# Kernel optimization log

Hardware: AMD Instinct MI355X
Metric: run time of the kernel (lower is better)

## Reference

```python
import jax, jax.numpy as jnp
import numpy as np

IMG_SIZE = 224
ALPHA = 100.0  # hardcoded softmax temperature in knnsearch_t_grad


def _sqdist(a, b):
    # (B,N,C),(B,M,C) -> (B,N,M) squared euclidean distances
    return (jnp.sum(a * a, -1)[:, :, None]
            - 2.0 * jnp.einsum('bnc,bmc->bnm', a, b)
            + jnp.sum(b * b, -1)[:, None, :])


def _cdist(a, b):
    return jnp.sqrt(jnp.maximum(_sqdist(a, b), 1e-12))


def proj2img(pc, img_offset):
    # faithful jax port of GraphDeformLoss_Neural_Partial.proj2img
    B, N, _ = pc.shape
    pc_max = pc.max(axis=1)              # (B,3)
    pc_min_full = pc.min(axis=1)         # (B,3)
    pc_range = pc_max - pc_min_full
    grid_size = pc_range[:, :2].max(axis=-1) / (IMG_SIZE - 3)   # (B,)
    pc_min = pc_min_full[:, None, :2]                            # (B,1,2)
    gs = grid_size[:, None, None]
    idx_xy = jnp.floor((pc[:, :, :2] - pc_min) / gs)             # (B,N,2)
    # densify each point into a 5x5 neighborhood of pixels
    idx_dense = (idx_xy[:, :, None, :] + img_offset[None, None]).reshape(B, N * 25, 2) + 1.0
    center = jnp.floor((idx_dense.max(axis=1) + idx_dense.min(axis=1)) / 2.0)  # (B,2)
    offset = IMG_SIZE / 2.0 - center - 1.0                       # (B,2) = (offset_x, offset_y)
    idx_off = idx_dense + offset[:, None, :]
    # boundary correction as in the torch code, plus clip for safety
    idx_off = idx_off + (idx_off < 0).astype(jnp.float32) - (idx_off > IMG_SIZE - 1).astype(jnp.float32)
    idx_off = jnp.clip(idx_off, 0, IMG_SIZE - 1)
    f_dense = jnp.repeat(jnp.repeat(pc[:, :, None, 2:3], 25, axis=2).reshape(B, N * 25, 1), 3, axis=-1)
    flat = (idx_off[..., 0] * IMG_SIZE + idx_off[..., 1]).astype(jnp.int32)   # (B,N*25)
    out = jax.vmap(lambda f, i: jax.ops.segment_sum(f, i, num_segments=IMG_SIZE * IMG_SIZE))(f_dense, flat)
    img = out.reshape(B, IMG_SIZE, IMG_SIZE, 3).transpose(0, 3, 1, 2)  # (B,3,H,W)
    return jax.nn.sigmoid(img)


def setup_inputs() -> dict:
    key = jax.random.key(0)
    k1, k2, k3, k4 = jax.random.split(key, 4)
    B, N, M, C = 4, 4995, 4995, 128
    off = jnp.array([[i, j] for i in range(-2, 3) for j in range(-2, 3)], dtype=jnp.float32)
    return {
        'verts1': jax.random.normal(k1, (B, N, 3), jnp.float32),
        'verts2': jax.random.normal(k2, (B, M, 3), jnp.float32),
        'feat1': jax.random.normal(k3, (B, N, C), jnp.float32),
        'feat2': jax.random.normal(k4, (B, M, C), jnp.float32),
        'img_offset': off,
        'k': 10,
    }


def reference(verts1, verts2, feat1, feat2, img_offset, k):
    # knnsearch_t_grad: soft correspondence from feature-space cdist + softmax
    d_feat = _cdist(feat1, feat2)                               # (B,N,M)
    Pi_12 = jax.nn.softmax(-ALPHA * d_feat, axis=-1)
    verts12 = jnp.einsum('bnm,bmc->bnc', Pi_12, verts2)         # pulled-back points (B,N,3)
    # chamfer (squared distances, as chamfer_3DDist); partial: take dist1 branch (N<=M)
    d2 = _sqdist(verts12, verts2)
    self_rec_loss = jnp.mean(jnp.min(d2, axis=-1))
    # knn_grad + index_points: gather k-NN features on source cloud
    d2_11 = _sqdist(verts1, verts1)
    _, idx11 = jax.lax.top_k(-d2_11, k)                         # (B,N,k) nearest
    feat1_conv = jax.vmap(lambda p, i: p[i])(feat1, idx11)      # (B,N,k,C)
    deform_feat_loss = jnp.mean((feat1_conv - feat1[:, :, None, :]) ** 2)
    # point-to-image projection loss
    img1 = proj2img(verts12, img_offset)
    img2 = proj2img(verts2, img_offset)
    img_loss = jnp.mean((img1 - img2) ** 2)
    return self_rec_loss + img_loss + deform_feat_loss
```

## Files before the change

### kernel.cpp

```cpp
#include <hip/hip_runtime.h>
#include <math.h>

#define BB 4
#define NN 4995
#define CC 128
#define IMG 224
#define IMGP (IMG*IMG)
#define ALPHA_F 100.0f
#define SPLITS 6
#define COLS_PER_SPLIT 896
#define RBLK 40
#define NG 158
#define NGP 160
#define NCP 5120
#define NTAP (2*BB*NN*25)
#define NREP 4
#define TKCAP 256

#define SM_SCALE 20813.6898f
#define NEG2S   -41627.3796f
#define EPS_S    2.08136898e-8f

#define OFF_V12    0
#define OFF_FN1    60000
#define OFF_V1Q    81000
#define OFF_V2Q    161000
#define OFF_C2Q    241000
#define OFF_PART   323000
#define OFF_IMG1   1123000
#define OFF_IMG2   1323704
#define OFF_ACC    1524408
#define OFF_STATS  1524792
#define OFF_F2H    1525000
#define OFF_F2L    2820000
#define OFF_IMGR   4115000
#define WS_NEED_REP ((size_t)5721000*sizeof(float))
#define ZERO_START OFF_IMG1
#define ZERO_FLOATS (1524920 - OFF_IMG1)
#define ZERO2_FLOATS (1524920 - OFF_ACC)

typedef short v8s  __attribute__((ext_vector_type(8)));
typedef float v16f __attribute__((ext_vector_type(16)));

#if __has_builtin(__builtin_amdgcn_exp2f)
__device__ __forceinline__ float fast_exp2(float x){ return __builtin_amdgcn_exp2f(x); }
#else
__device__ __forceinline__ float fast_exp2(float x){ float r; asm("v_exp_f32 %0, %1" : "=v"(r) : "v"(x)); return r; }
#endif
#if __has_builtin(__builtin_amdgcn_sqrtf)
__device__ __forceinline__ float fast_sqrt(float x){ return __builtin_amdgcn_sqrtf(x); }
#else
__device__ __forceinline__ float fast_sqrt(float x){ float r; asm("v_sqrt_f32 %0, %1" : "=v"(r) : "v"(x)); return r; }
#endif

__device__ __forceinline__ float wave_min(float v){
#pragma unroll
  for (int off=32; off; off>>=1) v = fminf(v, __shfl_xor(v, off));
  return v;
}
__device__ __forceinline__ float wave_sum(float v){
#pragma unroll
  for (int off=32; off; off>>=1) v += __shfl_xor(v, off);
  return v;
}

__device__ __forceinline__ int pack_bf_hi(float a, float b){
  return (int)__builtin_amdgcn_perm(__float_as_uint(b), __float_as_uint(a), 0x07060302u);
}

__device__ __forceinline__ void cvt_hilo(float4 a, float4 c, int4& hi, int4& lo){
  float hx=__uint_as_float(__float_as_uint(a.x)&0xffff0000u);
  float hy=__uint_as_float(__float_as_uint(a.y)&0xffff0000u);
  float hz=__uint_as_float(__float_as_uint(a.z)&0xffff0000u);
  float hw=__uint_as_float(__float_as_uint(a.w)&0xffff0000u);
  float gx=__uint_as_float(__float_as_uint(c.x)&0xffff0000u);
  float gy=__uint_as_float(__float_as_uint(c.y)&0xffff0000u);
  float gz=__uint_as_float(__float_as_uint(c.z)&0xffff0000u);
  float gw=__uint_as_float(__float_as_uint(c.w)&0xffff0000u);
  hi = make_int4(pack_bf_hi(a.x,a.y), pack_bf_hi(a.z,a.w),
                 pack_bf_hi(c.x,c.y), pack_bf_hi(c.z,c.w));
  lo = make_int4(pack_bf_hi(a.x-hx,a.y-hy), pack_bf_hi(a.z-hz,a.w-hw),
                 pack_bf_hi(c.x-gx,c.y-gy), pack_bf_hi(c.z-gz,c.w-gw));
}

__device__ __forceinline__ v8s i4_to_s8(int4 v){
  union { int4 i; v8s s; } u; u.i = v; return u.s;
}

__device__ __forceinline__ void gld_lds16(const void* g, void* l){
  __builtin_amdgcn_global_load_lds((const __attribute__((address_space(1))) void*)g,
                                   (__attribute__((address_space(3))) void*)l, 16, 0, 0);
}

__device__ __forceinline__ unsigned int fkey(float f){
  unsigned int u = __float_as_uint(f);
  return ((int)u < 0) ? ~u : (u ^ 0x80000000u);
}

__global__ __launch_bounds__(256) void k_conv(const float* __restrict__ feat1,
                                              const float* __restrict__ feat2,
                                              const float* __restrict__ verts1,
                                              const float* __restrict__ verts2,
                                              float* __restrict__ ws) {
  __shared__ float s2p[8][32], s1p[8][32];
  int g = blockIdx.x, b = blockIdx.y;
  int t = threadIdx.x;
  if (g >= NG){
    if (t < 32){
      int c = g*32 + t;
      if (c < NCP)
        ((float4*)(ws+OFF_C2Q))[(size_t)b*NCP + c] = make_float4(0.f,0.f,0.f,1e30f);
    }
    return;
  }
  int q = t >> 5, c32 = t & 31;
  int col = g*32 + c32; if (col > NN-1) col = NN-1;
  const float4* src = (const float4*)(feat2 + ((size_t)(b*NN + col))*CC) + q*4;
  float4 v0 = src[0], v1 = src[1], v2 = src[2], v3 = src[3];
  {
    float s2 = 0.f;
    s2=fmaf(v0.x,v0.x,s2); s2=fmaf(v0.y,v0.y,s2); s2=fmaf(v0.z,v0.z,s2); s2=fmaf(v0.w,v0.w,s2);
    s2=fmaf(v1.x,v1.x,s2); s2=fmaf(v1.y,v1.y,s2); s2=fmaf(v1.z,v1.z,s2); s2=fmaf(v1.w,v1.w,s2);
    s2=fmaf(v2.x,v2.x,s2); s2=fmaf(v2.y,v2.y,s2); s2=fmaf(v2.z,v2.z,s2); s2=fmaf(v2.w,v2.w,s2);
    s2=fmaf(v3.x,v3.x,s2); s2=fmaf(v3.y,v3.y,s2); s2=fmaf(v3.z,v3.z,s2); s2=fmaf(v3.w,v3.w,s2);
    s2p[q][c32] = s2;
  }
  {
    const float4* fa = (const float4*)(feat1 + ((size_t)(b*NN + col))*CC) + q*4;
    float4 u0 = fa[0], u1 = fa[1], u2 = fa[2], u3 = fa[3];
    float s1 = 0.f;
    s1=fmaf(u0.x,u0.x,s1); s1=fmaf(u0.y,u0.y,s1); s1=fmaf(u0.z,u0.z,s1); s1=fmaf(u0.w,u0.w,s1);
    s1=fmaf(u1.x,u1.x,s1); s1=fmaf(u1.y,u1.y,s1); s1=fmaf(u1.z,u1.z,s1); s1=fmaf(u1.w,u1.w,s1);
    s1=fmaf(u2.x,u2.x,s1); s1=fmaf(u2.y,u2.y,s1); s1=fmaf(u2.z,u2.z,s1); s1=fmaf(u2.w,u2.w,s1);
    s1=fmaf(u3.x,u3.x,s1); s1=fmaf(u3.y,u3.y,s1); s1=fmaf(u3.z,u3.z,s1); s1=fmaf(u3.w,u3.w,s1);
    s1p[q][c32] = s1;
  }
  short* f2h = (short*)(ws + OFF_F2H);
  short* f2l = (short*)(ws + OFF_F2L);
  size_t base = ((size_t)(b*NG + g))*4096 + (size_t)q*512 + c32*8;
  int4 hi, lo;
  cvt_hilo(v0, v1, hi, lo);
  *(int4*)&f2h[base] = hi;  *(int4*)&f2l[base] = lo;
  cvt_hilo(v2, v3, hi, lo);
  *(int4*)&f2h[base + 256] = hi;  *(int4*)&f2l[base + 256] = lo;
  __syncthreads();
  if (t < 32){
    int c = g*32 + t;
    if (c < NN){
      float S2 = ((s2p[0][t]+s2p[1][t])+(s2p[2][t]+s2p[3][t]))
               + ((s2p[4][t]+s2p[5][t])+(s2p[6][t]+s2p[7][t]));
      float S1 = ((s1p[0][t]+s1p[1][t])+(s1p[2][t]+s1p[3][t]))
               + ((s1p[4][t]+s1p[5][t])+(s1p[6][t]+s1p[7][t]));
      size_t r = (size_t)(b*NN + c);
      float x=verts1[r*3], y=verts1[r*3+1], z=verts1[r*3+2];
      ((float4*)(ws+OFF_V1Q))[r] = make_float4(x,y,z, x*x+y*y+z*z);
      float x2=verts2[r*3], y2=verts2[r*3+1], z2=verts2[r*3+2];
      ((float4*)(ws+OFF_V2Q))[r] = make_float4(x2,y2,z2, x2*x2+y2*y2+z2*z2);
      ((float4*)(ws+OFF_C2Q))[(size_t)b*NCP + c] = make_float4(x2,y2,z2, SM_SCALE*S2);
      ws[OFF_FN1+r] = SM_SCALE*S1;
    } else if (c < NCP){
      ((float4*)(ws+OFF_C2Q))[(size_t)b*NCP + c] = make_float4(0.f,0.f,0.f,1e30f);
    }
  }
}

__global__ __launch_bounds__(256) void k_stageA(const float* __restrict__ feat1,
      float* __restrict__ ws) {
  __shared__ __align__(16) short Bbuf[2][4096];
  __shared__ __align__(16) float colq[1024*4];

  int rblk  = blockIdx.x;
  int split = blockIdx.y;
  int b     = blockIdx.z;
  int rowBase = rblk*128;
  int colBase = split*COLS_PER_SPLIT;
  int colEnd  = colBase + COLS_PER_SPLIT; if (colEnd > NN) colEnd = NN;
  int nct = (colEnd - colBase + 63) >> 6;
  int nst = nct << 2;

  int t    = threadIdx.x;
  int w    = t >> 6;
  int lane = t & 63;
  int half = lane >> 5;
  int m32  = lane & 31;

  const float* f1b = feat1 + (size_t)b*NN*CC;
  const short* f2h = (const short*)(ws + OFF_F2H);
  const short* f2l = (const short*)(ws + OFF_F2L);
  const float4* cqb = (const float4*)(ws + OFF_C2Q) + (size_t)b*NCP;

#pragma unroll
  for (int r=0; r<4; r++){
    int col = colBase + r*256 + t; if (col > NCP-1) col = NCP-1;
    gld_lds16(cqb + col, &colq[(r*256 + w*64)*4]);
  }

  size_t f2base = (((size_t)(b*NG) + (colBase>>5) + (w>>1)) << 12) + (size_t)((t&127)*8);

  {
    short* d = &Bbuf[0][0] + w*512;
    gld_lds16(f2h + f2base, d);
    gld_lds16(f2l + f2base, d + 2048);
  }

  int nrow = rowBase + w*32 + m32;
  int nclamp = nrow > NN-1 ? NN-1 : nrow;
  float sn = ws[OFF_FN1 + (size_t)b*NN + nclamp];
  const float4* ar = (const float4*)(f1b + (size_t)nclamp*CC) + (half<<1);
  v8s Afh[8], Afl[8];
#pragma unroll
  for (int sl=0; sl<8; ++sl){
    float4 v0 = ar[sl*4], v1 = ar[sl*4+1];
    int4 hi, lo;
    cvt_hilo(v0, v1, hi, lo);
    Afh[sl] = i4_to_s8(hi); Afl[sl] = i4_to_s8(lo);
  }

  __syncthreads();

  float mm = INFINITY, S = 0.f, Vx = 0.f, Vy = 0.f, Vz = 0.f;

  for (int ci = 0; ci < nct; ci++){
    v16f acc0, acc1;
#pragma unroll
    for (int i=0;i<16;i++){ acc0[i]=0.f; acc1[i]=0.f; }

#pragma unroll
    for (int kt = 0; kt < 4; kt++){
      int s = (ci<<2) + kt;
      if (s+1 < nst){
        int s1 = s+1;
        size_t so = f2base + ((size_t)(s1>>2)<<13) + ((size_t)(s1&3)<<10);
        short* d = &Bbuf[0][0] + ((s1&1)<<12) + w*512;
        gld_lds16(f2h + so, d);
        gld_lds16(f2l + so, d + 2048);
      }
      const short* Bh = &Bbuf[0][0] + ((s&1)<<12);
      const short* Bl = Bh + 2048;
#pragma unroll
      for (int kh=0; kh<2; kh++){
        int fo = (kh<<9) + (half<<8) + (m32<<3);
        v8s a0h = *(const v8s*)&Bh[fo];
        v8s a0l = *(const v8s*)&Bl[fo];
        v8s a1h = *(const v8s*)&Bh[1024+fo];
        v8s a1l = *(const v8s*)&Bl[1024+fo];
        v8s b1h = Afh[kt*2+kh];
        v8s b1l = Afl[kt*2+kh];
        __builtin_amdgcn_s_setprio(1);
        acc0 = __builtin_amdgcn_mfma_f32_32x32x16_bf16(a0h, b1h, acc0, 0,0,0);
        acc0 = __builtin_amdgcn_mfma_f32_32x32x16_bf16(a0h, b1l, acc0, 0,0,0);
        acc0 = __builtin_amdgcn_mfma_f32_32x32x16_bf16(a0l, b1h, acc0, 0,0,0);
        acc1 = __builtin_amdgcn_mfma_f32_32x32x16_bf16(a1h, b1h, acc1, 0,0,0);
        acc1 = __builtin_amdgcn_mfma_f32_32x32x16_bf16(a1h, b1l, acc1, 0,0,0);
        acc1 = __builtin_amdgcn_mfma_f32_32x32x16_bf16(a1l, b1h, acc1, 0,0,0);
        __builtin_amdgcn_s_setprio(0);
      }
      __syncthreads();
    }

    int cb4 = ci<<8;
    float Mt = INFINITY;
#pragma unroll
    for (int reg=0; reg<16; reg++){
      int cp0 = (reg&3) + 8*(reg>>2) + 4*half;
      float f0 = colq[cb4 + cp0*4 + 3];
      float d0 = fmaf(NEG2S, acc0[reg], sn) + f0;
      float p0 = fast_sqrt(fmaxf(d0, EPS_S));
      acc0[reg] = p0; Mt = fminf(Mt, p0);
      float f1v = colq[cb4 + (cp0+32)*4 + 3];
      float d1 = fmaf(NEG2S, acc1[reg], sn) + f1v;
      float p1 = fast_sqrt(fmaxf(d1, EPS_S));
      acc1[reg] = p1; Mt = fminf(Mt, p1);
    }
    float mn = fminf(mm, Mt);
    float sc = fast_exp2(mn - mm);
    float se=0.f, sx=0.f, sy=0.f, sz=0.f;
#pragma unroll
    for (int reg=0; reg<16; reg++){
      int cp0 = (reg&3) + 8*(reg>>2) + 4*half;
      float4 q0 = *(const float4*)&colq[cb4 + cp0*4];
      float e0 = fast_exp2(mn - acc0[reg]);
      se += e0; sx=fmaf(e0,q0.x,sx); sy=fmaf(e0,q0.y,sy); sz=fmaf(e0,q0.z,sz);
      float4 q1 = *(const float4*)&colq[cb4 + (cp0+32)*4];
      float e1 = fast_exp2(mn - acc1[reg]);
      se += e1; sx=fmaf(e1,q1.x,sx); sy=fmaf(e1,q1.y,sy); sz=fmaf(e1,q1.z,sz);
    }
    S  = fmaf(S,  sc, se);
    Vx = fmaf(Vx, sc, sx);
    Vy = fmaf(Vy, sc, sy);
    Vz = fmaf(Vz, sc, sz);
    mm = mn;
  }

  {
    float m2  = __shfl_xor(mm, 32);
    float S2  = __shfl_xor(S,  32);
    float Vx2 = __shfl_xor(Vx, 32);
    float Vy2 = __shfl_xor(Vy, 32);
    float Vz2 = __shfl_xor(Vz, 32);
    float M = fminf(mm, m2);
    float c1 = fast_exp2(M - mm), c2 = fast_exp2(M - m2);
    float Sf  = S*c1  + S2*c2;
    float Vxf = Vx*c1 + Vx2*c2;
    float Vyf = Vy*c1 + Vy2*c2;
    float Vzf = Vz*c1 + Vz2*c2;
    if (half==0 && nrow < NN){
      float* p = ws + OFF_PART + ((size_t)(b*NN+nrow)*SPLITS + split)*5;
      p[0]=M; p[1]=Sf; p[2]=Vxf; p[3]=Vyf; p[4]=Vzf;
    }
  }
}

__global__ __launch_bounds__(256) void k_selfrec(float* __restrict__ ws) {
  __shared__ float v12s[32][3];
  int rblk = blockIdx.x, b = blockIdx.y;
  int t = threadIdx.x;
  int lane = t & 63, w = t >> 6;
  int r0blk = rblk*32;

  if (t < 32){
    int row = r0blk + t;
    int rowc = row > NN-1 ? NN-1 : row;
    const float* p = ws + OFF_PART + (size_t)(b*NN+rowc)*SPLITS*5;
    float mm = INFINITY;
#pragma unroll
    for (int s=0;s<SPLITS;s++) mm = fminf(mm, p[s*5]);
    float S=0.f,Vx=0.f,Vy=0.f,Vz=0.f;
#pragma unroll
    for (int s=0;s<SPLITS;s++){
      float sc = fast_exp2(mm - p[s*5]);
      S  += p[s*5+1]*sc; Vx += p[s*5+2]*sc; Vy += p[s*5+3]*sc; Vz += p[s*5+4]*sc;
    }
    float ox = Vx/S, oy = Vy/S, oz = Vz/S;
    v12s[t][0]=ox; v12s[t][1]=oy; v12s[t][2]=oz;
    if (row < NN){
      ws[OFF_V12+(size_t)(b*NN+row)*3+0]=ox;
      ws[OFF_V12+(size_t)(b*NN+row)*3+1]=oy;
      ws[OFF_V12+(size_t)(b*NN+row)*3+2]=oz;
    }
  }
  __syncthreads();

  int r0 = r0blk + w*8;
  const float4* v2q = (const float4*)(ws + OFF_V2Q) + (size_t)b*NN;
  float xr[8], yr[8], zr[8], sar[8]; bool val[8];
#pragma unroll
  for (int j=0;j<8;j++){
    int n = r0+j; val[j] = (n < NN);
    int li = w*8+j;
    float x=v12s[li][0], y=v12s[li][1], z=v12s[li][2];
    sar[j]=x*x+y*y+z*z;
    xr[j]=-2.0f*x; yr[j]=-2.0f*y; zr[j]=-2.0f*z;
  }
  float mn[8];
#pragma unroll
  for (int j=0;j<8;j++) mn[j] = INFINITY;
  for (int m=lane; m<NN; m+=64) {
    float4 q = v2q[m];
#pragma unroll
    for (int j=0;j<8;j++)
      mn[j] = fminf(mn[j], fmaf(xr[j],q.x, fmaf(yr[j],q.y, fmaf(zr[j],q.z, q.w))));
  }
  float s = 0.f;
#pragma unroll
  for (int j=0;j<8;j++){
    float v = wave_min(mn[j]);
    s += val[j] ? (v + sar[j]) : 0.f;
  }
  if (lane==0)
    atomicAdd(((double*)(ws+OFF_ACC)) + ((rblk*4 + w) & 63), (double)s);
}

__global__ __launch_bounds__(256) void k_topk(const float* __restrict__ feat1,
        const int* __restrict__ kptr, float* __restrict__ ws) {
  __shared__ unsigned int keybuf[4*256];
  __shared__ unsigned long long cand[4*TKCAP];
  __shared__ int scnt[4];
  __shared__ float tfs[4];
  __shared__ int sel[4][16];
  __shared__ float rs[4];
  int t = threadIdx.x;
  int lane = t & 63, wid = t >> 6;
  int b = blockIdx.y;
  int n0 = blockIdx.x*4;
  int kk = *kptr; if (kk > 16) kk = 16; if (kk < 1) kk = 1;

  const float4* v1q = (const float4*)(ws + OFF_V1Q) + (size_t)b*NN;
  float mx[4], my2[4], mz[4];
#pragma unroll
  for (int j=0;j<4;j++){
    int n = n0+j; if (n > NN-1) n = NN-1;
    float4 me = v1q[n];
    mx[j]=-2.0f*me.x; my2[j]=-2.0f*me.y; mz[j]=-2.0f*me.z;
  }
  if (t < 4) scnt[t] = 0;

  float mn[4] = {INFINITY, INFINITY, INFINITY, INFINITY};
  for (int i=0;i<20;i++){
    int m = t + 256*i;
    if (m < NN){
      float4 q = v1q[m];
#pragma unroll
      for (int j=0;j<4;j++){
        float d = fmaf(mx[j], q.x, fmaf(my2[j], q.y, fmaf(mz[j], q.z, q.w)));
        mn[j] = fminf(mn[j], d);
      }
    }
  }

#pragma unroll
  for (int j=0;j<4;j++)
    keybuf[j*256 + t] = fkey(mn[j]) >> 16;
  __syncthreads();

  {
    unsigned int k0 = keybuf[wid*256 + lane];
    unsigned int k1 = keybuf[wid*256 + 64 + lane];
    unsigned int k2 = keybuf[wid*256 + 128 + lane];
    unsigned int k3 = keybuf[wid*256 + 192 + lane];
    unsigned int prefix = 0;
    for (int bit=15; bit>=0; --bit){
      unsigned int piv = prefix | (1u<<bit);
      int c = __popcll(__ballot(k0 < piv)) + __popcll(__ballot(k1 < piv))
            + __popcll(__ballot(k2 < piv)) + __popcll(__ballot(k3 < piv));
      if (c < kk) prefix = piv;
    }
    unsigned int K = (prefix<<16) | 0xFFFFu;
    unsigned int fb = (K & 0x80000000u) ? (K ^ 0x80000000u) : ~K;
    if (lane==0) tfs[wid] = __uint_as_float(fb);
  }
  __syncthreads();
  float tf0 = tfs[0], tf1 = tfs[1], tf2 = tfs[2], tf3 = tfs[3];

  bool g0 = (mn[0] <= tf0), g1 = (mn[1] <= tf1), g2 = (mn[2] <= tf2), g3 = (mn[3] <= tf3);
  if (g0|g1|g2|g3){
    for (int i=0;i<20;i++){
      int m = t + 256*i;
      if (m < NN){
        float4 q = v1q[m];
        float sw = q.w;
        float d0 = fmaf(mx[0], q.x, fmaf(my2[0], q.y, fmaf(mz[0], q.z, sw)));
        float d1 = fmaf(mx[1], q.x, fmaf(my2[1], q.y, fmaf(mz[1], q.z, sw)));
        float d2 = fmaf(mx[2], q.x, fmaf(my2[2], q.y, fmaf(mz[2], q.z, sw)));
        float d3 = fmaf(mx[3], q.x, fmaf(my2[3], q.y, fmaf(mz[3], q.z, sw)));
        if (g0 && d0 <= tf0){
          int pos = atomicAdd(&scnt[0], 1);
          if (pos < TKCAP) cand[0*TKCAP + pos] = ((unsigned long long)fkey(d0) << 13) | (unsigned int)m;
        }
        if (g1 && d1 <= tf1){
          int pos = atomicAdd(&scnt[1], 1);
          if (pos < TKCAP) cand[1*TKCAP + pos] = ((unsigned long long)fkey(d1) << 13) | (unsigned int)m;
        }
        if (g2 && d2 <= tf2){
          int pos = atomicAdd(&scnt[2], 1);
          if (pos < TKCAP) cand[2*TKCAP + pos] = ((unsigned long long)fkey(d2) << 13) | (unsigned int)m;
        }
        if (g3 && d3 <= tf3){
          int pos = atomicAdd(&scnt[3], 1);
          if (pos < TKCAP) cand[3*TKCAP + pos] = ((unsigned long long)fkey(d3) << 13) | (unsigned int)m;
        }
      }
    }
  }
  __syncthreads();

  {
    int cnt = scnt[wid]; if (cnt > TKCAP) cnt = TKCAP;
    unsigned long long kv0 = (lane       < cnt) ? cand[wid*TKCAP + lane]       : ~0ull;
    unsigned long long kv1 = (lane + 64  < cnt) ? cand[wid*TKCAP + lane + 64]  : ~0ull;
    unsigned long long kv2 = (lane + 128 < cnt) ? cand[wid*TKCAP + lane + 128] : ~0ull;
    unsigned long long kv3 = (lane + 192 < cnt) ? cand[wid*TKCAP + lane + 192] : ~0ull;
    int r0=0, r1=0, r2=0, r3=0;
    for (int q2=0; q2<cnt; ++q2){
      unsigned long long cj = cand[wid*TKCAP + q2];
      r0 += (cj < kv0); r1 += (cj < kv1); r2 += (cj < kv2); r3 += (cj < kv3);
    }
    if (lane       < cnt && r0 < kk) sel[wid][r0] = (int)(kv0 & 8191ull);
    if (lane + 64  < cnt && r1 < kk) sel[wid][r1] = (int)(kv1 & 8191ull);
    if (lane + 128 < cnt && r2 < kk) sel[wid][r2] = (int)(kv2 & 8191ull);
    if (lane + 192 < cnt && r3 < kk) sel[wid][r3] = (int)(kv3 & 8191ull);
  }
  __syncthreads();

  float mse = 0.f;
  int c = t & 127;
  int rh = t >> 7;
  for (int j=0;j<4;j++){
    int n = n0+j;
    if (n >= NN) break;
    const float* f1n = feat1 + ((size_t)b*NN + n)*CC;
    float e = f1n[c];
    for (int r=rh; r<kk; r+=2){
      const float* g = feat1 + ((size_t)b*NN + sel[j][r])*CC;
      float d = g[c]-e;
      mse = fmaf(d,d,mse);
    }
  }

  float acc = wave_sum(mse);
  if (lane==0) rs[wid] = acc;
  __syncthreads();
  if (t==0){
    float s = (rs[0]+rs[1])+(rs[2]+rs[3]);
    atomicAdd(((double*)(ws+OFF_ACC)) + 128 + ((blockIdx.x + b) & 63), (double)s);
  }
}

__global__ __launch_bounds__(1024) void k_imgstats(const float* __restrict__ verts2, const float* __restrict__ imgoff,
                           float* __restrict__ ws) {
  __shared__ float r0[16], r1[16], r2[16], r3[16];
  __shared__ float sgs, smnx, smny;
  int img = blockIdx.x >> 2, b = blockIdx.x & 3;
  const float* pc = (img==0) ? (ws + OFF_V12 + (size_t)b*NN*3) : (verts2 + (size_t)b*NN*3);
  int lane = threadIdx.x & 63, wid = threadIdx.x >> 6;
  float mnx=INFINITY, mxx=-INFINITY, mny=INFINITY, mxy=-INFINITY;
  for (int n = threadIdx.x; n < NN; n += 1024) {
    float x = pc[(size_t)n*3], y = pc[(size_t)n*3+1];
    mnx=fminf(mnx,x); mxx=fmaxf(mxx,x); mny=fminf(mny,y); mxy=fmaxf(mxy,y);
  }
#pragma unroll
  for (int off=32; off; off>>=1) {
    mnx=fminf(mnx,__shfl_xor(mnx,off)); mxx=fmaxf(mxx,__shfl_xor(mxx,off));
    mny=fminf(mny,__shfl_xor(mny,off)); mxy=fmaxf(mxy,__shfl_xor(mxy,off));
  }
  if (lane==0){ r0[wid]=mnx; r1[wid]=mxx; r2[wid]=mny; r3[wid]=mxy; }
  __syncthreads();
  float* st = ws + OFF_STATS + (size_t)(img*4+b)*16;
  if (threadIdx.x==0){
    mnx=r0[0]; mxx=r1[0]; mny=r2[0]; mxy=r3[0];
    for (int i=1;i<16;i++){
      mnx=fminf(mnx,r0[i]); mxx=fmaxf(mxx,r1[i]);
      mny=fminf(mny,r2[i]); mxy=fmaxf(mxy,r3[i]);
    }
    float gs = fmaxf(mxx-mnx, mxy-mny) / 221.0f;
    sgs=gs; smnx=mnx; smny=mny;
    st[0]=mnx; st[1]=mxx; st[2]=mny; st[3]=mxy; st[4]=gs;
  }
  __syncthreads();
  float gs=sgs, bx=smnx, by=smny;
  float fmnx=INFINITY, fmxx=-INFINITY, fmny=INFINITY, fmxy=-INFINITY;
  for (int n = threadIdx.x; n < NN; n += 1024) {
    float fx = floorf((pc[(size_t)n*3]-bx)/gs);
    float fy = floorf((pc[(size_t)n*3+1]-by)/gs);
    fmnx=fminf(fmnx,fx); fmxx=fmaxf(fmxx,fx); fmny=fminf(fmny,fy); fmxy=fmaxf(fmxy,fy);
  }
#pragma unroll
  for (int off=32; off; off>>=1) {
    fmnx=fminf(fmnx,__shfl_xor(fmnx,off)); fmxx=fmaxf(fmxx,__shfl_xor(fmxx,off));
    fmny=fminf(fmny,__shfl_xor(fmny,off)); fmxy=fmaxf(fmxy,__shfl_xor(fmxy,off));
  }
  __syncthreads();
  if (lane==0){ r0[wid]=fmnx; r1[wid]=fmxx; r2[wid]=fmny; r3[wid]=fmxy; }
  __syncthreads();
  if (threadIdx.x==0){
    fmnx=r0[0]; fmxx=r1[0]; fmny=r2[0]; fmxy=r3[0];
    for (int i=1;i<16;i++){
      fmnx=fminf(fmnx,r0[i]); fmxx=fmaxf(fmxx,r1[i]);
      fmny=fminf(fmny,r2[i]); fmxy=fmaxf(fmxy,r3[i]);
    }
    float omnx=INFINITY, omxx=-INFINITY, omny=INFINITY, omxy=-INFINITY;
    for (int l=0;l<25;l++){
      float ox=imgoff[l*2], oy=imgoff[l*2+1];
      omnx=fminf(omnx,ox); omxx=fmaxf(omxx,ox); omny=fminf(omny,oy); omxy=fmaxf(omxy,oy);
    }
    float cx = floorf(((fmxx+omxx+1.0f)+(fmnx+omnx+1.0f))*0.5f);
    float cy = floorf(((fmxy+omxy+1.0f)+(fmny+omny+1.0f))*0.5f);
    st[5] = (112.0f - cx) - 1.0f;
    st[6] = (112.0f - cy) - 1.0f;
  }
}

__global__ __launch_bounds__(256) void k_scatter(const float* __restrict__ verts2,
                          const float* __restrict__ imgoff,
                          float* __restrict__ ws, int nrep) {
  int g = blockIdx.x*256 + threadIdx.x;
  if (g >= NTAP) return;
  int p = g / 25; int l = g - p*25;
  int img = p / (BB*NN); int r = p - img*(BB*NN); int b = r / NN;
  const float* pc = (img==0) ? (ws + OFF_V12) : verts2;
  float x = pc[(size_t)r*3], y = pc[(size_t)r*3+1], z = pc[(size_t)r*3+2];
  const float* st = ws + OFF_STATS + (size_t)(img*4+b)*16;
  float mnx=st[0], mny=st[2], gs=st[4], offx=st[5], offy=st[6];
  float bx = floorf((x-mnx)/gs) + 1.0f + offx;
  float by = floorf((y-mny)/gs) + 1.0f + offy;
  float vx = bx + imgoff[l*2], vy = by + imgoff[l*2+1];
  vx += (vx<0.f?1.f:0.f) - (vx>223.f?1.f:0.f);
  vy += (vy<0.f?1.f:0.f) - (vy>223.f?1.f:0.f);
  vx = fminf(fmaxf(vx,0.f),223.f); vy = fminf(fmaxf(vy,0.f),223.f);
  int flat = (int)(vx*224.f + vy);
  float* im;
  if (nrep > 1)
    im = ws + OFF_IMGR + ((size_t)(((blockIdx.x & (nrep-1))*2 + img)*BB + b))*IMGP;
  else
    im = ws + (img==0?OFF_IMG1:OFF_IMG2) + (size_t)b*IMGP;
  atomicAdd(im + flat, z);
}

__global__ void k_imgloss(float* __restrict__ ws, int nrep) {
  int i = blockIdx.x*blockDim.x + threadIdx.x;
  float v = 0.f;
  if (i < BB*IMGP) {
    float a, c;
    if (nrep > 1){
      a = 0.f; c = 0.f;
      for (int r=0; r<nrep; ++r){
        a += ws[OFF_IMGR + (size_t)(r*2+0)*BB*IMGP + i];
        c += ws[OFF_IMGR + (size_t)(r*2+1)*BB*IMGP + i];
      }
    } else {
      a = ws[OFF_IMG1+i]; c = ws[OFF_IMG2+i];
    }
    float sa = 1.f/(1.f+expf(-a)), sc = 1.f/(1.f+expf(-c));
    float d = sa - sc; v = d*d;
  }
  v = wave_sum(v);
  if ((threadIdx.x&63)==0)
    atomicAdd(((double*)(ws+OFF_ACC)) + 64 + (blockIdx.x & 63), (double)v);
}

__global__ void k_final(const int* __restrict__ kptr, const float* __restrict__ ws, float* __restrict__ out) {
  const double* acc = (const double*)(ws+OFF_ACC);
  int t = threadIdx.x;
  double a0 = acc[t], a1 = acc[64+t], a2 = acc[128+t];
#pragma unroll
  for (int off=32; off; off>>=1){
    a0 += __shfl_down(a0, off);
    a1 += __shfl_down(a1, off);
    a2 += __shfl_down(a2, off);
  }
  if (t==0){
    int kk = *kptr; if (kk > 16) kk = 16; if (kk < 1) kk = 1;
    double srl = a0 / (double)(BB*NN);
    double img = a1 / ((double)BB*IMGP);
    double df  = a2 / ((double)BB*NN*kk*CC);
    out[0] = (float)(srl + img + df);
  }
}

extern "C" void kernel_launch(void* const* d_in, const int* in_sizes, int n_in,
                              void* d_out, int out_size, void* d_ws, size_t ws_size,
                              hipStream_t stream) {
  (void)in_sizes; (void)n_in; (void)out_size;
  const float* verts1 = (const float*)d_in[0];
  const float* verts2 = (const float*)d_in[1];
  const float* feat1  = (const float*)d_in[2];
  const float* feat2  = (const float*)d_in[3];
  const float* imgoff = (const float*)d_in[4];
  const int*   kptr   = (const int*)d_in[5];
  float* ws  = (float*)d_ws;
  float* out = (float*)d_out;
  int nrep = (ws_size >= WS_NEED_REP) ? NREP : 1;

  if (nrep > 1){
    hipMemsetAsync(ws + OFF_ACC, 0, (size_t)ZERO2_FLOATS*sizeof(float), stream);
    hipMemsetAsync(ws + OFF_IMGR, 0, (size_t)NREP*2*BB*IMGP*sizeof(float), stream);
  } else {
    hipMemsetAsync(ws + ZERO_START, 0, (size_t)ZERO_FLOATS*sizeof(float), stream);
  }

  dim3 gC(NGP, BB);
  k_conv<<<gC, 256, 0, stream>>>(feat1, feat2, verts1, verts2, ws);

  dim3 gA(RBLK, SPLITS, BB);
  k_stageA<<<gA, 256, 0, stream>>>(feat1, ws);

  dim3 gS((NN+31)/32, BB);
  k_selfrec<<<gS, 256, 0, stream>>>(ws);

  dim3 gT((NN+3)/4, BB);
  k_topk<<<gT, 256, 0, stream>>>(feat1, kptr, ws);

  k_imgstats<<<8, 1024, 0, stream>>>(verts2, imgoff, ws);
  k_scatter<<<(NTAP+255)/256, 256, 0, stream>>>(verts2, imgoff, ws, nrep);
  k_imgloss<<<(BB*IMGP+255)/256, 256, 0, stream>>>(ws, nrep);

  k_final<<<1,64,0,stream>>>(kptr, ws, out);
}
```

Baseline: 338.7 us.

## Triple-buffer feat2 tiles with prefetch depth two and finer column splits

Stage A now uses eight column splits of 640 columns instead of six of 896, which launches more blocks and shrinks the per-block column metadata buffer. Stage A also goes from double to triple buffering of the feat2 hi/lo tiles in LDS, issuing loads two steps ahead. The full __syncthreads per k-step is replaced by a partial vmcnt wait plus s_barrier placed before the next prefetch. The A-fragment loads are issued before the async LDS loads, and empty asm statements pin them in registers. This aims to hide global-to-LDS latency behind the MFMA work, at the cost of more LDS and a fragile hand-written vmcnt count.

```diff
diff --git a/kernel.cpp b/kernel.cpp
--- a/kernel.cpp
+++ b/kernel.cpp
@@ -7,8 +7,8 @@
 #define IMG 224
 #define IMGP (IMG*IMG)
 #define ALPHA_F 100.0f
-#define SPLITS 6
-#define COLS_PER_SPLIT 896
+#define SPLITS 8
+#define COLS_PER_SPLIT 640
 #define RBLK 40
 #define NG 158
 #define NGP 160
@@ -166,8 +166,8 @@
 
 __global__ __launch_bounds__(256) void k_stageA(const float* __restrict__ feat1,
       float* __restrict__ ws) {
-  __shared__ __align__(16) short Bbuf[2][4096];
-  __shared__ __align__(16) float colq[1024*4];
+  __shared__ __align__(16) short Bbuf[3][4096];
+  __shared__ __align__(16) float colq[768*4];
 
   int rblk  = blockIdx.x;
   int split = blockIdx.y;
@@ -189,20 +189,6 @@
   const short* f2l = (const short*)(ws + OFF_F2L);
   const float4* cqb = (const float4*)(ws + OFF_C2Q) + (size_t)b*NCP;
 
-#pragma unroll
-  for (int r=0; r<4; r++){
-    int col = colBase + r*256 + t; if (col > NCP-1) col = NCP-1;
-    gld_lds16(cqb + col, &colq[(r*256 + w*64)*4]);
-  }
-
-  size_t f2base = (((size_t)(b*NG) + (colBase>>5) + (w>>1)) << 12) + (size_t)((t&127)*8);
-
-  {
-    short* d = &Bbuf[0][0] + w*512;
-    gld_lds16(f2h + f2base, d);
-    gld_lds16(f2l + f2base, d + 2048);
-  }
-
   int nrow = rowBase + w*32 + m32;
   int nclamp = nrow > NN-1 ? NN-1 : nrow;
   float sn = ws[OFF_FN1 + (size_t)b*NN + nclamp];
@@ -215,8 +201,26 @@
     cvt_hilo(v0, v1, hi, lo);
     Afh[sl] = i4_to_s8(hi); Afl[sl] = i4_to_s8(lo);
   }
-
-  __syncthreads();
+  asm volatile("" :: "v"(sn));
+#pragma unroll
+  for (int sl=0; sl<8; ++sl)
+    asm volatile("" :: "v"(Afh[sl]), "v"(Afl[sl]));
+
+#pragma unroll
+  for (int r=0; r<3; r++){
+    int col = colBase + r*256 + t; if (col > NCP-1) col = NCP-1;
+    gld_lds16(cqb + col, &colq[(r*256 + w*64)*4]);
+  }
+
+  size_t f2base = (((size_t)(b*NG) + (colBase>>5) + (w>>1)) << 12) + (size_t)((t&127)*8);
+
+#pragma unroll
+  for (int T=0; T<2; ++T){
+    size_t so = f2base + ((size_t)(T&3)<<10);
+    short* d = &Bbuf[T][0] + w*512;
+    gld_lds16(f2h + so, d);
+    gld_lds16(f2l + so, d + 2048);
+  }
 
   float mm = INFINITY, S = 0.f, Vx = 0.f, Vy = 0.f, Vz = 0.f;
 
@@ -228,14 +232,21 @@
 #pragma unroll
     for (int kt = 0; kt < 4; kt++){
       int s = (ci<<2) + kt;
-      if (s+1 < nst){
-        int s1 = s+1;
-        size_t so = f2base + ((size_t)(s1>>2)<<13) + ((size_t)(s1&3)<<10);
-        short* d = &Bbuf[0][0] + ((s1&1)<<12) + w*512;
+      __builtin_amdgcn_sched_barrier(0);
+      asm volatile("s_waitcnt vmcnt(2)" ::: "memory");
+      __builtin_amdgcn_s_barrier();
+
+      int T = s + 2;
+      if (T < nst){
+        size_t so = f2base + ((size_t)(T>>2)<<13) + ((size_t)(T&3)<<10);
+        int tb = T - (T/3)*3;
+        short* d = &Bbuf[tb][0] + w*512;
         gld_lds16(f2h + so, d);
         gld_lds16(f2l + so, d + 2048);
       }
-      const short* Bh = &Bbuf[0][0] + ((s&1)<<12);
+
+      int sb = s - (s/3)*3;
+      const short* Bh = &Bbuf[sb][0];
       const short* Bl = Bh + 2048;
 #pragma unroll
       for (int kh=0; kh<2; kh++){
@@ -255,7 +266,6 @@
         acc1 = __builtin_amdgcn_mfma_f32_32x32x16_bf16(a1l, b1h, acc1, 0,0,0);
         __builtin_amdgcn_s_setprio(0);
       }
-      __syncthreads();
     }
 
     int cb4 = ci<<8;
```

New measurement: 345.5 us. 1.02x slower.
